# Kernel tuning notes

Measured on AMD Instinct MI355X. Metric: run time of the kernel, lower is better.

The kernel has to match this reference:

```python
import jax, jax.numpy as jnp
import numpy as np

N = 16384       # input points
D_IN = 64       # feature dim
D_OUT = 128     # output dim
STRIDE = 4      # downsampling stride -> M = N // STRIDE sampled points
NSAMPLE = 16    # hard-coded in __init__
BN_EPS = 1e-5


def setup_inputs() -> dict:
    key = jax.random.key(0)
    k1, k2, k3 = jax.random.split(key, 3)
    p = jax.random.normal(k1, (N, 3), jnp.float32)
    x = jax.random.normal(k2, (N, D_IN), jnp.float32)
    o = jnp.array([N], jnp.int32)  # single-cloud offsets
    # mlp params: Linear(d_in+3, d_out) + BatchNorm1d(d_out)
    W = jax.random.normal(k3, (D_IN + 3, D_OUT), jnp.float32) * 0.05
    b = jnp.zeros((D_OUT,), jnp.float32)
    gamma = jnp.ones((D_OUT,), jnp.float32)
    beta = jnp.zeros((D_OUT,), jnp.float32)
    return {"p": p, "x": x, "o": o, "W": W, "b": b, "gamma": gamma, "beta": beta}


def fps(p, m):
    """Furthest point sampling: returns m indices into p [N,3]. Sequential by nature."""
    n = p.shape[0]
    dists = jnp.full((n,), jnp.inf, p.dtype)
    idxs = jnp.zeros((m,), jnp.int32)  # start from point 0 (pointops convention)

    def body(i, carry):
        idxs, dists = carry
        last = p[idxs[i - 1]]                      # [3]
        d = jnp.sum((p - last) ** 2, axis=1)       # [N]
        dists = jnp.minimum(dists, d)
        return idxs.at[i].set(jnp.argmax(dists).astype(jnp.int32)), dists

    idxs, _ = jax.lax.fori_loop(1, m, body, (idxs, dists))
    return idxs


def reference(p, x, o, W, b, gamma, beta):
    m = p.shape[0] // STRIDE  # static
    # --- furthest point sampling (non-differentiable index op, as in pointops) ---
    s_idx = fps(jax.lax.stop_gradient(p), m)
    n_p = p[s_idx]                                             # [M,3]
    # --- query-and-group: kNN of each sampled point over all N points ---
    d2 = (jnp.sum(n_p ** 2, axis=1)[:, None]
          + jnp.sum(p ** 2, axis=1)[None, :]
          - 2.0 * n_p @ p.T)                                   # [M,N]
    _, nn_idx = jax.lax.top_k(-d2, NSAMPLE)                    # [M,K]
    pj = p[nn_idx] - n_p[:, None, :]                           # [M,K,3] relative coords
    xj = x[nn_idx]                                             # [M,K,D_IN]
    # normalize relative coords by max neighbor norm per sampled point
    nrm = jnp.linalg.norm(pj, axis=-1, keepdims=True)          # [M,K,1]
    pj = pj / (jnp.max(nrm, axis=1, keepdims=True) + 1e-8)
    feat = jnp.concatenate([pj, xj], axis=-1).max(axis=1)      # [M, 3+D_IN] max-pool
    # --- MLP: Linear + BatchNorm1d (training stats) + ReLU ---
    h = feat @ W + b                                           # [M, D_OUT]
    mean = jnp.mean(h, axis=0)
    var = jnp.var(h, axis=0)
    h = (h - mean) / jnp.sqrt(var + BN_EPS) * gamma + beta
    x_out = jax.nn.relu(h)
    n_o = jnp.array([m], jnp.int32)
    return (n_p, x_out, n_o)
```

## Files before the change

kernel.cpp:

```cpp
#include <hip/hip_runtime.h>

#define N_PTS 16384
#define M_PTS 4096
#define D_INF 64
#define D_OUTF 128
#define KNN 16
#define DF 67

__global__ __launch_bounds__(256) void sp_kernel(const float* __restrict__ p,
                                                 float* __restrict__ spn) {
  int j = blockIdx.x * 256 + threadIdx.x;
  float a = p[3 * j], b = p[3 * j + 1], c = p[3 * j + 2];
  spn[j] = __fadd_rn(__fadd_rn(__fmul_rn(a, a), __fmul_rn(b, b)), __fmul_rn(c, c));
}

#define FPS_T 1024
#define FPS_W (FPS_T / 64)

#define REP16(F) F(0) F(1) F(2) F(3) F(4) F(5) F(6) F(7) \
                 F(8) F(9) F(10) F(11) F(12) F(13) F(14) F(15)

__global__ __launch_bounds__(FPS_T, 4) void fps_kernel(const float* __restrict__ p,
                                                       int* __restrict__ sidx,
                                                       float* __restrict__ np_out) {
  const int t = threadIdx.x;
  const int lane = t & 63;
  const int wave = t >> 6;

#define FPS_DECL(k) float px##k, py##k, pz##k, dd##k;
  REP16(FPS_DECL)
#define FPS_LOAD(k) { int j = t + (k << 10); \
    px##k = p[3 * j]; py##k = p[3 * j + 1]; pz##k = p[3 * j + 2]; \
    dd##k = INFINITY; }
  REP16(FPS_LOAD)

  __shared__ unsigned long long s_key[2][FPS_W];

  float lx = p[0], ly = p[1], lz = p[2];
  if (t == 0) {
    sidx[0] = 0;
    np_out[0] = lx; np_out[1] = ly; np_out[2] = lz;
  }
  for (int i = 1; i < M_PTS; ++i) {
    const int bsel = i & 1;
    float bestv = -1.0f;
    int besti = 0;
#define FPS_STEP(k) { \
    float dx = __fsub_rn(px##k, lx); \
    float dy = __fsub_rn(py##k, ly); \
    float dz = __fsub_rn(pz##k, lz); \
    float d = __fadd_rn(__fadd_rn(__fmul_rn(dx, dx), __fmul_rn(dy, dy)), \
                        __fmul_rn(dz, dz)); \
    float nd = fminf(dd##k, d); \
    dd##k = nd; \
    if (nd > bestv) { bestv = nd; besti = t + (k << 10); } }
    REP16(FPS_STEP)
    unsigned long long key =
        ((unsigned long long)__float_as_uint(bestv) << 32) |
        (unsigned int)(~besti);
#pragma unroll
    for (int off = 32; off >= 1; off >>= 1) {
      unsigned long long ok = __shfl_xor(key, off);
      key = (ok > key) ? ok : key;
    }
    if (lane == 0) s_key[bsel][wave] = key;
    __syncthreads();
    unsigned long long kk = s_key[bsel][lane & (FPS_W - 1)];
#pragma unroll
    for (int off = 32; off >= 1; off >>= 1) {
      unsigned long long ok = __shfl_xor(kk, off);
      kk = (ok > kk) ? ok : kk;
    }
    int gi = (int)(~(unsigned int)kk);
    lx = p[3 * gi]; ly = p[3 * gi + 1]; lz = p[3 * gi + 2];
    if (t == 0) {
      sidx[i] = gi;
      np_out[3 * i] = lx; np_out[3 * i + 1] = ly; np_out[3 * i + 2] = lz;
    }
  }
}

__global__ __launch_bounds__(256) void knn_feat_kernel(const float* __restrict__ p,
                                                       const float* __restrict__ x,
                                                       const float* __restrict__ spn,
                                                       const int* __restrict__ sidx,
                                                       float* __restrict__ feat) {
  __shared__ float cd[4][256];
  __shared__ int ci[4][256];
  __shared__ int cnt[4];
  __shared__ int s_nn[4][KNN];
  const int w = threadIdx.x >> 6;
  const int lane = threadIdx.x & 63;
  const int q = (blockIdx.x << 2) + w;
  const int qi = sidx[q];
  const float qx = p[3 * qi], qy = p[3 * qi + 1], qz = p[3 * qi + 2];
  const float sn = spn[qi];
  if (lane == 0) cnt[w] = 0;
  float lmin = INFINITY;
  for (int it = 0; it < N_PTS / 64; ++it) {
    int j = lane + (it << 6);
    float dot = __fmaf_rn(qz, p[3 * j + 2],
                 __fmaf_rn(qy, p[3 * j + 1], __fmul_rn(qx, p[3 * j])));
    float d2 = __fsub_rn(__fadd_rn(sn, spn[j]), __fmul_rn(2.0f, dot));
    lmin = fminf(lmin, d2);
  }
  float mv = lmin;
  float tau = INFINITY;
#pragma unroll
  for (int r = 0; r < KNN; ++r) {
    float rmin = mv;
#pragma unroll
    for (int off = 32; off >= 1; off >>= 1) rmin = fminf(rmin, __shfl_xor(rmin, off));
    tau = rmin;
    unsigned long long msk = __ballot(mv == rmin);
    if (lane == (int)(__ffsll(msk) - 1)) mv = INFINITY;
  }
  __syncthreads();
  for (int it = 0; it < N_PTS / 64; ++it) {
    int j = lane + (it << 6);
    float dot = __fmaf_rn(qz, p[3 * j + 2],
                 __fmaf_rn(qy, p[3 * j + 1], __fmul_rn(qx, p[3 * j])));
    float d2 = __fsub_rn(__fadd_rn(sn, spn[j]), __fmul_rn(2.0f, dot));
    if (d2 <= tau) {
      int pos = atomicAdd(&cnt[w], 1);
      if (pos < 256) { cd[w][pos] = d2; ci[w][pos] = j; }
    }
  }
  __syncthreads();
  int C = min(cnt[w], 256);
  float vv[4]; int ii[4];
#pragma unroll
  for (int s = 0; s < 4; ++s) {
    int pos = lane + (s << 6);
    bool ok = pos < C;
    vv[s] = ok ? cd[w][pos] : INFINITY;
    ii[s] = ok ? ci[w][pos] : 0x7FFFFFFF;
  }
#pragma unroll
  for (int r = 0; r < KNN; ++r) {
    float bv = vv[0]; int bi = ii[0]; int bs = 0;
#pragma unroll
    for (int s = 1; s < 4; ++s) {
      bool tk = (vv[s] < bv) || (vv[s] == bv && ii[s] < bi);
      bv = tk ? vv[s] : bv; bi = tk ? ii[s] : bi; bs = tk ? s : bs;
    }
    float rv = bv; int ri = bi;
#pragma unroll
    for (int off = 32; off >= 1; off >>= 1) {
      float ov = __shfl_xor(rv, off); int oi = __shfl_xor(ri, off);
      bool tk = (ov < rv) || (ov == rv && oi < ri);
      rv = tk ? ov : rv; ri = tk ? oi : ri;
    }
    if (bi == ri) {
#pragma unroll
      for (int s = 0; s < 4; ++s) if (s == bs) vv[s] = INFINITY;
    }
    if (lane == 0) s_nn[w][r] = ri;
  }
  __syncthreads();
  float ax = -INFINITY, ay = -INFINITY, az = -INFINITY, nr = -INFINITY;
  if (lane < KNN) {
    int jn = s_nn[w][lane];
    ax = __fsub_rn(p[3 * jn], qx);
    ay = __fsub_rn(p[3 * jn + 1], qy);
    az = __fsub_rn(p[3 * jn + 2], qz);
    nr = sqrtf(__fadd_rn(__fadd_rn(__fmul_rn(ax, ax), __fmul_rn(ay, ay)),
                         __fmul_rn(az, az)));
  }
  float mnr = nr, mx = ax, my = ay, mz = az;
#pragma unroll
  for (int off = 32; off >= 1; off >>= 1) {
    mnr = fmaxf(mnr, __shfl_xor(mnr, off));
    mx = fmaxf(mx, __shfl_xor(mx, off));
    my = fmaxf(my, __shfl_xor(my, off));
    mz = fmaxf(mz, __shfl_xor(mz, off));
  }
  if (lane == 0) {
    float sden = __fadd_rn(mnr, 1e-8f);
    feat[q * DF + 0] = mx / sden;
    feat[q * DF + 1] = my / sden;
    feat[q * DF + 2] = mz / sden;
  }
  float fm = -INFINITY;
#pragma unroll
  for (int k = 0; k < KNN; ++k) {
    int jn = s_nn[w][k];
    fm = fmaxf(fm, x[(jn << 6) + lane]);
  }
  feat[q * DF + 3 + lane] = fm;
}

__global__ __launch_bounds__(128) void mlp_kernel(const float* __restrict__ feat,
                                                  const float* __restrict__ W,
                                                  const float* __restrict__ b,
                                                  float* __restrict__ h) {
  int mrow = blockIdx.x;
  int o = threadIdx.x;
  const float* fr = feat + mrow * DF;
  float acc = b[o];
#pragma unroll
  for (int k = 0; k < DF; ++k) acc = __fmaf_rn(fr[k], W[k * D_OUTF + o], acc);
  h[mrow * D_OUTF + o] = acc;
}

__global__ __launch_bounds__(256) void stats_kernel(const float* __restrict__ h,
                                                    const float* __restrict__ gamma,
                                                    const float* __restrict__ beta,
                                                    float* __restrict__ scsh) {
  int o = blockIdx.x;
  int t = threadIdx.x;
  float s = 0.f, s2 = 0.f;
  for (int mrow = t; mrow < M_PTS; mrow += 256) {
    float v = h[mrow * D_OUTF + o];
    s += v;
    s2 = __fmaf_rn(v, v, s2);
  }
#pragma unroll
  for (int off = 32; off >= 1; off >>= 1) {
    s += __shfl_xor(s, off);
    s2 += __shfl_xor(s2, off);
  }
  __shared__ float as1[4], as2[4];
  if ((t & 63) == 0) { as1[t >> 6] = s; as2[t >> 6] = s2; }
  __syncthreads();
  if (t == 0) {
    float ts = ((as1[0] + as1[1]) + as1[2]) + as1[3];
    float ts2 = ((as2[0] + as2[1]) + as2[2]) + as2[3];
    float mean = ts / (float)M_PTS;
    float var = ts2 / (float)M_PTS - mean * mean;
    var = fmaxf(var, 0.f);
    float sc = gamma[o] / sqrtf(var + 1e-5f);
    scsh[o] = sc;
    scsh[D_OUTF + o] = beta[o] - mean * sc;
  }
}

__global__ __launch_bounds__(256) void bn_kernel(const float* __restrict__ h,
                                                 const float* __restrict__ scsh,
                                                 float* __restrict__ out) {
  int idx = blockIdx.x * 256 + threadIdx.x;
  int o = idx & (D_OUTF - 1);
  float v = __fmaf_rn(h[idx], scsh[o], scsh[D_OUTF + o]);
  out[M_PTS * 3 + idx] = fmaxf(v, 0.f);
  if (idx == 0) out[M_PTS * 3 + M_PTS * D_OUTF] = 4096.0f;
}

extern "C" void kernel_launch(void* const* d_in, const int* in_sizes, int n_in,
                              void* d_out, int out_size, void* d_ws, size_t ws_size,
                              hipStream_t stream) {
  const float* p     = (const float*)d_in[0];
  const float* x     = (const float*)d_in[1];
  const float* W     = (const float*)d_in[3];
  const float* b     = (const float*)d_in[4];
  const float* gamma = (const float*)d_in[5];
  const float* beta  = (const float*)d_in[6];
  float* out = (float*)d_out;

  float* wsf  = (float*)d_ws;
  int*   sidx = (int*)d_ws;
  float* spn  = wsf + 4096;
  float* feat = spn + N_PTS;
  float* h    = feat + M_PTS * DF;
  float* scsh = h + M_PTS * D_OUTF;

  sp_kernel<<<N_PTS / 256, 256, 0, stream>>>(p, spn);
  fps_kernel<<<1, FPS_T, 0, stream>>>(p, sidx, out);
  knn_feat_kernel<<<M_PTS / 4, 256, 0, stream>>>(p, x, spn, sidx, feat);
  mlp_kernel<<<M_PTS, D_OUTF, 0, stream>>>(feat, W, b, h);
  stats_kernel<<<D_OUTF, 256, 0, stream>>>(h, gamma, beta, scsh);
  bn_kernel<<<(M_PTS * D_OUTF) / 256, 256, 0, stream>>>(h, scsh, out);
}
```

Baseline: 8.480 ms.

## Spatially bin points into chunks and prune FPS updates with bounding boxes

Points are sorted into a Morton-ordered grid of cells, packed into 64-point chunks with bounding boxes, and FPS then updates only chunks whose box lower bound can still shrink their max min-distance. This cuts per-iteration distance work from all N points to the dirty chunks. In exchange it adds several preprocessing kernels, keeps min-distances in global memory instead of registers, and adds an extra barrier per iteration. The chunk-skip test uses a 0.9999 slack factor, and the argmax tie-break depends on the original index stored in each point.

```diff
diff --git a/kernel.cpp b/kernel.cpp
--- a/kernel.cpp
+++ b/kernel.cpp
@@ -6,6 +6,8 @@
 #define D_OUTF 128
 #define KNN 16
 #define DF 67
+#define NCH 256
+#define NCELL 512
 
 __global__ __launch_bounds__(256) void sp_kernel(const float* __restrict__ p,
                                                  float* __restrict__ spn) {
@@ -14,60 +16,155 @@
   spn[j] = __fadd_rn(__fadd_rn(__fmul_rn(a, a), __fmul_rn(b, b)), __fmul_rn(c, c));
 }
 
-#define FPS_T 1024
-#define FPS_W (FPS_T / 64)
-
-#define REP16(F) F(0) F(1) F(2) F(3) F(4) F(5) F(6) F(7) \
-                 F(8) F(9) F(10) F(11) F(12) F(13) F(14) F(15)
-
-__global__ __launch_bounds__(FPS_T, 4) void fps_kernel(const float* __restrict__ p,
-                                                       int* __restrict__ sidx,
-                                                       float* __restrict__ np_out) {
+__device__ __forceinline__ int cell_of(float x, float y, float z) {
+  int qx = (int)floorf((x + 6.0f) * 0.6666667f);
+  int qy = (int)floorf((y + 6.0f) * 0.6666667f);
+  int qz = (int)floorf((z + 6.0f) * 0.6666667f);
+  qx = min(max(qx, 0), 7); qy = min(max(qy, 0), 7); qz = min(max(qz, 0), 7);
+  return (qx & 1) | ((qy & 1) << 1) | ((qz & 1) << 2)
+       | ((qx & 2) << 2) | ((qy & 2) << 3) | ((qz & 2) << 4)
+       | ((qx & 4) << 4) | ((qy & 4) << 5) | ((qz & 4) << 6);
+}
+
+__global__ __launch_bounds__(256) void hist_kernel(const float* __restrict__ p,
+                                                   int* __restrict__ hist) {
+  int j = blockIdx.x * 256 + threadIdx.x;
+  atomicAdd(&hist[cell_of(p[3 * j], p[3 * j + 1], p[3 * j + 2])], 1);
+}
+
+__global__ __launch_bounds__(NCELL) void scan_kernel(const int* __restrict__ hist,
+                                                     int* __restrict__ cellptr) {
+  __shared__ int sh[NCELL];
+  int t = threadIdx.x;
+  int self = hist[t];
+  sh[t] = self;
+  __syncthreads();
+  for (int off = 1; off < NCELL; off <<= 1) {
+    int v = sh[t];
+    int a = (t >= off) ? sh[t - off] : 0;
+    __syncthreads();
+    sh[t] = v + a;
+    __syncthreads();
+  }
+  cellptr[t] = sh[t] - self;
+}
+
+__global__ __launch_bounds__(256) void scatter_kernel(const float* __restrict__ p,
+                                                      int* __restrict__ cellptr,
+                                                      float4* __restrict__ sp4) {
+  int j = blockIdx.x * 256 + threadIdx.x;
+  float x = p[3 * j], y = p[3 * j + 1], z = p[3 * j + 2];
+  int pos = atomicAdd(&cellptr[cell_of(x, y, z)], 1);
+  sp4[pos] = make_float4(x, y, z, __int_as_float(j));
+}
+
+__global__ __launch_bounds__(64) void bbox_kernel(const float4* __restrict__ sp4,
+                                                  float* __restrict__ chunkbb) {
+  int c = blockIdx.x;
+  int lane = threadIdx.x;
+  float4 q = sp4[(c << 6) + lane];
+  float mnx = q.x, mxx = q.x, mny = q.y, mxy = q.y, mnz = q.z, mxz = q.z;
+#pragma unroll
+  for (int off = 32; off >= 1; off >>= 1) {
+    mnx = fminf(mnx, __shfl_xor(mnx, off)); mxx = fmaxf(mxx, __shfl_xor(mxx, off));
+    mny = fminf(mny, __shfl_xor(mny, off)); mxy = fmaxf(mxy, __shfl_xor(mxy, off));
+    mnz = fminf(mnz, __shfl_xor(mnz, off)); mxz = fmaxf(mxz, __shfl_xor(mxz, off));
+  }
+  if (lane == 0) {
+    chunkbb[8 * c + 0] = mnx; chunkbb[8 * c + 1] = mny; chunkbb[8 * c + 2] = mnz;
+    chunkbb[8 * c + 3] = mxx; chunkbb[8 * c + 4] = mxy; chunkbb[8 * c + 5] = mxz;
+  }
+}
+
+__global__ __launch_bounds__(1024) void fps2_kernel(const float* __restrict__ p,
+                                                    const float4* __restrict__ sp4,
+                                                    const float* __restrict__ chunkbb,
+                                                    float* __restrict__ dd,
+                                                    int* __restrict__ sidx,
+                                                    float* __restrict__ np_out) {
   const int t = threadIdx.x;
   const int lane = t & 63;
   const int wave = t >> 6;
-
-#define FPS_DECL(k) float px##k, py##k, pz##k, dd##k;
-  REP16(FPS_DECL)
-#define FPS_LOAD(k) { int j = t + (k << 10); \
-    px##k = p[3 * j]; py##k = p[3 * j + 1]; pz##k = p[3 * j + 2]; \
-    dd##k = INFINITY; }
-  REP16(FPS_LOAD)
-
-  __shared__ unsigned long long s_key[2][FPS_W];
-
+  __shared__ float s_bb[NCH * 9];
+  __shared__ float s_ddmax[NCH];
+  __shared__ unsigned long long s_key[NCH];
+  __shared__ unsigned short s_dirty[NCH];
+  __shared__ int s_cnt[2];
+  __shared__ unsigned long long s_wkey[2][16];
+
+  for (int j = t; j < N_PTS; j += 1024) dd[j] = INFINITY;
+  if (t < NCH) {
+#pragma unroll
+    for (int k = 0; k < 6; ++k) s_bb[9 * t + k] = chunkbb[8 * t + k];
+    s_ddmax[t] = INFINITY;
+  }
   float lx = p[0], ly = p[1], lz = p[2];
   if (t == 0) {
+    s_cnt[0] = 0; s_cnt[1] = 0;
     sidx[0] = 0;
     np_out[0] = lx; np_out[1] = ly; np_out[2] = lz;
   }
+  __syncthreads();
+
   for (int i = 1; i < M_PTS; ++i) {
-    const int bsel = i & 1;
-    float bestv = -1.0f;
-    int besti = 0;
-#define FPS_STEP(k) { \
-    float dx = __fsub_rn(px##k, lx); \
-    float dy = __fsub_rn(py##k, ly); \
-    float dz = __fsub_rn(pz##k, lz); \
-    float d = __fadd_rn(__fadd_rn(__fmul_rn(dx, dx), __fmul_rn(dy, dy)), \
-                        __fmul_rn(dz, dz)); \
-    float nd = fminf(dd##k, d); \
-    dd##k = nd; \
-    if (nd > bestv) { bestv = nd; besti = t + (k << 10); } }
-    REP16(FPS_STEP)
-    unsigned long long key =
-        ((unsigned long long)__float_as_uint(bestv) << 32) |
-        (unsigned int)(~besti);
+    const int buf = i & 1;
+    if (t < NCH) {
+      float ax = fmaxf(fmaxf(__fsub_rn(s_bb[9 * t + 0], lx),
+                             __fsub_rn(lx, s_bb[9 * t + 3])), 0.f);
+      float ay = fmaxf(fmaxf(__fsub_rn(s_bb[9 * t + 1], ly),
+                             __fsub_rn(ly, s_bb[9 * t + 4])), 0.f);
+      float az = fmaxf(fmaxf(__fsub_rn(s_bb[9 * t + 2], lz),
+                             __fsub_rn(lz, s_bb[9 * t + 5])), 0.f);
+      float lb2 = __fadd_rn(__fadd_rn(__fmul_rn(ax, ax), __fmul_rn(ay, ay)),
+                            __fmul_rn(az, az));
+      if (__fmul_rn(lb2, 0.9999f) < s_ddmax[t]) {
+        int pos = atomicAdd(&s_cnt[buf], 1);
+        s_dirty[pos] = (unsigned short)t;
+      }
+    }
+    __syncthreads();
+    const int cnt = s_cnt[buf];
+    if (t == 0) s_cnt[buf ^ 1] = 0;
+    const int rounds = (cnt + 15) >> 4;
+    for (int r = 0; r < rounds; ++r) {
+      int li = (r << 4) + wave;
+      if (li < cnt) {
+        int c = s_dirty[li];
+        int pos = (c << 6) + lane;
+        float4 q = sp4[pos];
+        float dx = __fsub_rn(q.x, lx);
+        float dy = __fsub_rn(q.y, ly);
+        float dz = __fsub_rn(q.z, lz);
+        float d = __fadd_rn(__fadd_rn(__fmul_rn(dx, dx), __fmul_rn(dy, dy)),
+                            __fmul_rn(dz, dz));
+        float nd = fminf(dd[pos], d);
+        dd[pos] = nd;
+        unsigned long long key =
+            ((unsigned long long)__float_as_uint(nd) << 32) |
+            (unsigned int)(~__float_as_int(q.w));
+#pragma unroll
+        for (int off = 32; off >= 1; off >>= 1) {
+          unsigned long long ok = __shfl_xor(key, off);
+          key = (ok > key) ? ok : key;
+        }
+        if (lane == 0) {
+          s_key[c] = key;
+          s_ddmax[c] = __uint_as_float((unsigned int)(key >> 32));
+        }
+      }
+    }
+    __syncthreads();
+    unsigned long long k2 = (t < NCH) ? s_key[t] : 0ull;
 #pragma unroll
     for (int off = 32; off >= 1; off >>= 1) {
-      unsigned long long ok = __shfl_xor(key, off);
-      key = (ok > key) ? ok : key;
-    }
-    if (lane == 0) s_key[bsel][wave] = key;
-    __syncthreads();
-    unsigned long long kk = s_key[bsel][lane & (FPS_W - 1)];
-#pragma unroll
-    for (int off = 32; off >= 1; off >>= 1) {
+      unsigned long long ok = __shfl_xor(k2, off);
+      k2 = (ok > k2) ? ok : k2;
+    }
+    if (lane == 0) s_wkey[buf][wave] = k2;
+    __syncthreads();
+    unsigned long long kk = s_wkey[buf][lane & 15];
+#pragma unroll
+    for (int off = 8; off >= 1; off >>= 1) {
       unsigned long long ok = __shfl_xor(kk, off);
       kk = (ok > kk) ? ok : kk;
     }
@@ -262,9 +359,19 @@
   float* feat = spn + N_PTS;
   float* h    = feat + M_PTS * DF;
   float* scsh = h + M_PTS * D_OUTF;
+  int*    hist    = (int*)feat;
+  int*    cellptr = hist + 512;
+  float4* sp4     = (float4*)h;
+  float*  chunkbb = h + N_PTS * 4;
+  float*  dd      = chunkbb + NCH * 8;
 
   sp_kernel<<<N_PTS / 256, 256, 0, stream>>>(p, spn);
-  fps_kernel<<<1, FPS_T, 0, stream>>>(p, sidx, out);
+  hipMemsetAsync(hist, 0, NCELL * sizeof(int), stream);
+  hist_kernel<<<N_PTS / 256, 256, 0, stream>>>(p, hist);
+  scan_kernel<<<1, NCELL, 0, stream>>>(hist, cellptr);
+  scatter_kernel<<<N_PTS / 256, 256, 0, stream>>>(p, cellptr, sp4);
+  bbox_kernel<<<NCH, 64, 0, stream>>>(sp4, chunkbb);
+  fps2_kernel<<<1, 1024, 0, stream>>>(p, sp4, chunkbb, dd, sidx, out);
   knn_feat_kernel<<<M_PTS / 4, 256, 0, stream>>>(p, x, spn, sidx, feat);
   mlp_kernel<<<M_PTS, D_OUTF, 0, stream>>>(feat, W, b, h);
   stats_kernel<<<D_OUTF, 256, 0, stream>>>(h, gamma, beta, scsh);
```

Result: slower. 11.33 ms (+33.6%).
